# Kernel tuning notes

Hardware: AMD Instinct MI355X
Metric: run time of the kernel (lower is better)

Reference implementation:

```python
import jax, jax.numpy as jnp
import numpy as np

N_PTS = 2000   # n: number of Z1 samples (rows of K_Z1Z1)
Z_PTS = 2000   # z: number of Z2 samples (cols of K_Z1Z2 / gammas)
A_SAMP = 1000  # a: number of alpha samples
D = 8          # d: treatment dimension


def setup_inputs() -> dict:
    key = jax.random.key(0)
    ks = jax.random.split(key, 8)
    M = jax.random.normal(ks[0], (N_PTS, D), jnp.float32)
    N = jax.random.normal(ks[1], (N_PTS, D), jnp.float32)
    X = (M + N) / 2  # initial_X in the torch module (the nn.Parameter)
    # PSD kernel matrix so the ridge solve is well conditioned
    A = jax.random.normal(ks[2], (N_PTS, N_PTS), jnp.float32)
    K_Z1Z1 = (A @ A.T) / N_PTS
    K_Z1Z2 = jax.random.normal(ks[3], (N_PTS, Z_PTS), jnp.float32) * 0.1
    gamma_MN = jax.random.normal(ks[4], (N_PTS, Z_PTS), jnp.float32) * 0.01
    # offset keeps the complex denominator exps @ gamma_N away from zero
    gamma_N = jax.random.normal(ks[5], (N_PTS, Z_PTS), jnp.float32) * 0.01 + 1.0 / N_PTS
    alpha_samples = jax.random.normal(ks[6], (A_SAMP, D), jnp.float32)
    log_lambda_X = jnp.zeros((1,), jnp.float32)  # log(lambda_N) with lambda_N = 1.0
    return {
        "M": M, "N": N, "X": X, "log_lambda_X": log_lambda_X,
        "K_Z1Z1": K_Z1Z1, "K_Z1Z2": K_Z1Z2,
        "gamma_MN": gamma_MN, "gamma_N": gamma_N,
        "alpha_samples": alpha_samples,
    }


def _compute_labels(alpha, exponent, gamma_num, gamma_den, mult_num):
    # exps: [a, n] complex64 phase features exp(i * <alpha, exponent_j>)
    exps = jnp.exp(1j * (alpha @ exponent.T))
    # denominator: [a, z]
    denom = exps @ gamma_den.astype(jnp.complex64)
    # numerator: [a, z, d]
    num = jnp.einsum('jd,jz,aj->azd',
                     mult_num.astype(jnp.complex64),
                     gamma_num.astype(jnp.complex64),
                     exps)
    return num / denom[:, :, None]


def reference(M, N, X, log_lambda_X, K_Z1Z1, K_Z1Z2, gamma_MN, gamma_N, alpha_samples):
    n = K_Z1Z1.shape[0]
    # kernel ridge solve: gamma_X = (K + n*exp(log_lambda)*I)^{-1} K_Z1Z2  -> [n, z]
    reg = n * jnp.exp(log_lambda_X[0])
    gamma_X = jnp.linalg.solve(K_Z1Z1 + reg * jnp.eye(n, dtype=K_Z1Z1.dtype), K_Z1Z2)
    MN_labels = _compute_labels(alpha_samples, N, gamma_MN, gamma_N, M)   # [a, z, d]
    X_labels = _compute_labels(alpha_samples, X, gamma_X, gamma_X, X)     # [a, z, d]
    diff = MN_labels - X_labels
    # torch.linalg.norm(., dim=-1)**2 on complex == sum |.|^2 over d
    loss = jnp.mean(jnp.sum(jnp.abs(diff) ** 2, axis=-1))
    return loss
```

## Files before the change

### kernel.cpp

```cpp
#include <hip/hip_runtime.h>


typedef __bf16 bf16;
typedef __bf16 bf16x8 __attribute__((ext_vector_type(8)));
typedef float f32x4 __attribute__((ext_vector_type(4)));
typedef int i32x8 __attribute__((ext_vector_type(8)));

#define AS1 __attribute__((address_space(1)))
#define AS3 __attribute__((address_space(3)))

__device__ __forceinline__ void async16(const void* g, void* l) {
  __builtin_amdgcn_global_load_lds((AS1 const unsigned int*)g,
                                   (AS3 unsigned int*)l, 16, 0, 0);
}

__device__ __forceinline__ unsigned int pk4f8(float a, float b, float c,
                                              float d) {
  int w = __builtin_amdgcn_cvt_pk_fp8_f32(a, b, 0, false);
  w = __builtin_amdgcn_cvt_pk_fp8_f32(c, d, w, true);
  return (unsigned int)w;
}

__device__ __forceinline__ void build_mn(const float* __restrict__ gMN,
                                         const float* __restrict__ Mm,
                                         unsigned char* __restrict__ B8,
                                         int j0, int zl0, int zg0, int ZC,
                                         int tid, float (*t)[65]) {
  const size_t PL = (size_t)ZC * 2048;
  int zg = zg0 + zl0;
  for (int e = tid; e < 4096; e += 256) {
    int r = e >> 6, c = e & 63;
    t[r][c] = (j0 + r < 2000 && zg + c < 2000)
                  ? gMN[(size_t)(j0 + r) * 2000 + zg + c] : 0.f;
  }
  __syncthreads();
  const float4* M4 = (const float4*)Mm;
#pragma unroll
  for (int it = 0; it < 2; ++it) {
    int idx = it * 256 + tid;
    int zr = idx >> 3, c8 = (idx & 7) * 8;
    float g[8], mrow[8][8];
#pragma unroll
    for (int e = 0; e < 8; ++e) {
      g[e] = 64.f * t[c8 + e][zr];
      int jj = j0 + c8 + e;
      if (jj < 2000) {
        float4 ma = M4[jj * 2], mb = M4[jj * 2 + 1];
        mrow[e][0] = ma.x; mrow[e][1] = ma.y; mrow[e][2] = ma.z;
        mrow[e][3] = ma.w; mrow[e][4] = mb.x; mrow[e][5] = mb.y;
        mrow[e][6] = mb.z; mrow[e][7] = mb.w;
      } else {
#pragma unroll
        for (int d = 0; d < 8; ++d) mrow[e][d] = 0.f;
      }
    }
    size_t ob = (size_t)(zl0 + zr) * 2048 + j0 + c8;
#pragma unroll
    for (int d = 0; d < 8; ++d) {
      uint2 u;
      u.x = pk4f8(g[0] * mrow[0][d], g[1] * mrow[1][d], g[2] * mrow[2][d],
                  g[3] * mrow[3][d]);
      u.y = pk4f8(g[4] * mrow[4][d], g[5] * mrow[5][d], g[6] * mrow[6][d],
                  g[7] * mrow[7][d]);
      *(uint2*)(B8 + (size_t)d * PL + ob) = u;
    }
  }
}

__device__ __forceinline__ void build_x(const bf16* __restrict__ gxHi,
                                        const bf16* __restrict__ gxLo,
                                        const float* __restrict__ Xm,
                                        unsigned char* __restrict__ B8,
                                        int j0, int zl0, int zg0, int ZC,
                                        int tid) {
  const size_t PL = (size_t)ZC * 2048;
  const float4* X4 = (const float4*)Xm;
#pragma unroll
  for (int it = 0; it < 2; ++it) {
    int idx = it * 256 + tid;
    int zr = idx >> 3, c8 = (idx & 7) * 8;
    size_t gb = (size_t)(zg0 + zl0 + zr) * 2048 + j0 + c8;
    bf16x8 vh = *(const bf16x8*)(gxHi + gb);
    bf16x8 vl = *(const bf16x8*)(gxLo + gb);
    float gx[8], xr[8][8];
#pragma unroll
    for (int e = 0; e < 8; ++e) {
      gx[e] = 8192.f * ((float)vh[e] + (float)vl[e]);
      int jj = j0 + c8 + e;
      if (jj < 2000) {
        float4 xa = X4[jj * 2], xb = X4[jj * 2 + 1];
        xr[e][0] = xa.x; xr[e][1] = xa.y; xr[e][2] = xa.z; xr[e][3] = xa.w;
        xr[e][4] = xb.x; xr[e][5] = xb.y; xr[e][6] = xb.z; xr[e][7] = xb.w;
      } else {
#pragma unroll
        for (int d = 0; d < 8; ++d) xr[e][d] = 0.f;
      }
    }
    size_t ob = (size_t)(zl0 + zr) * 2048 + j0 + c8;
#pragma unroll
    for (int d = 0; d < 8; ++d) {
      uint2 u;
      u.x = pk4f8(gx[0] * xr[0][d], gx[1] * xr[1][d], gx[2] * xr[2][d],
                  gx[3] * xr[3][d]);
      u.y = pk4f8(gx[4] * xr[4][d], gx[5] * xr[5][d], gx[6] * xr[6][d],
                  gx[7] * xr[7][d]);
      *(uint2*)(B8 + (size_t)(8 + d) * PL + ob) = u;
    }
  }
}

__global__ __launch_bounds__(256) void k_cvt(
    const float* __restrict__ K11, const float* __restrict__ K12,
    const float* __restrict__ gN, bf16* __restrict__ Kbf,
    bf16* __restrict__ K12T, bf16* __restrict__ K12TL,
    bf16* __restrict__ BtNh, bf16* __restrict__ BtNl,
    float* __restrict__ out) {
  __shared__ float t[64][65];
  const int bid = blockIdx.x, tid = threadIdx.x;
  if (bid < 2048) {
    if (bid == 0 && tid == 0) out[0] = 0.f;
    int e = (bid * 256 + tid) * 8;
    int j = e >> 11, k = e & 2047;
    bf16x8 v;
    if (j < 2000 && k < 2000) {
      const float4* s = (const float4*)(K11 + (size_t)j * 2000 + k);
      float4 f0 = s[0], f1 = s[1];
      v[0] = (bf16)f0.x; v[1] = (bf16)f0.y; v[2] = (bf16)f0.z; v[3] = (bf16)f0.w;
      v[4] = (bf16)f1.x; v[5] = (bf16)f1.y; v[6] = (bf16)f1.z; v[7] = (bf16)f1.w;
    } else {
      for (int i = 0; i < 8; ++i) v[i] = (bf16)0.f;
    }
    *(bf16x8*)(Kbf + e) = v;
  } else {
    bool isK12 = bid < 3072;
    const float* src = isK12 ? K12 : gN;
    bf16* dh = isK12 ? K12T : BtNh;
    bf16* dl = isK12 ? K12TL : BtNl;
    int b2 = bid - (isK12 ? 2048 : 3072);
    int j0 = (b2 & 31) * 64, z0 = (b2 >> 5) * 64;
    for (int e = tid; e < 4096; e += 256) {
      int r = e >> 6, c = e & 63;
      t[r][c] = (j0 + r < 2000 && z0 + c < 2000)
                    ? src[(size_t)(j0 + r) * 2000 + z0 + c] : 0.f;
    }
    __syncthreads();
#pragma unroll
    for (int it = 0; it < 2; ++it) {
      int idx = it * 256 + tid;
      int zr = idx >> 3, c8 = (idx & 7) * 8;
      bf16x8 vh, vl;
#pragma unroll
      for (int e = 0; e < 8; ++e) {
        float g = t[c8 + e][zr];
        bf16 h = (bf16)g;
        vh[e] = h;
        vl[e] = (bf16)(g - (float)h);
      }
      size_t ob = (size_t)(z0 + zr) * 2048 + j0 + c8;
      *(bf16x8*)(dh + ob) = vh;
      *(bf16x8*)(dl + ob) = vl;
    }
  }
}

__global__ __launch_bounds__(256, 2) void k_big(
    const bf16* __restrict__ K12T, const bf16* __restrict__ K12TL,
    const bf16* __restrict__ Kbf, const float* __restrict__ ll,
    const float* __restrict__ al, const float* __restrict__ Nm,
    const float* __restrict__ Xm, const float* __restrict__ gMN,
    const float* __restrict__ Mm, bf16* __restrict__ gxHi,
    bf16* __restrict__ gxLo, bf16* __restrict__ AphH,
    bf16* __restrict__ AphL, unsigned char* __restrict__ Aph8,
    unsigned char* __restrict__ B8, int ZC) {
  __shared__ __align__(16) char smem[34816];
  const int tid = threadIdx.x;
  const int bid = blockIdx.x;
  if (bid >= 1280) {
    int pid = bid - 1280;
    build_mn(gMN, Mm, B8, (pid & 31) * 64, (pid >> 5) * 64, 0, ZC, tid,
             (float(*)[65])smem);
    return;
  }
  if (bid >= 256) {
    const size_t PA = (size_t)1024 * 2048;
    int a = bid - 256;
    int j0 = tid * 8;
    float vc[4][8];
    if (a < 1000) {
      const float4* A4 = (const float4*)al;
      const float4* N4 = (const float4*)Nm;
      const float4* X4 = (const float4*)Xm;
      float4 a0 = A4[a * 2], a1 = A4[a * 2 + 1];
#pragma unroll
      for (int e = 0; e < 8; ++e) {
        int j = j0 + e;
        if (j < 2000) {
          float4 n0 = N4[j * 2], n1 = N4[j * 2 + 1];
          float4 x0 = X4[j * 2], x1 = X4[j * 2 + 1];
          float pn = a0.x * n0.x + a0.y * n0.y + a0.z * n0.z + a0.w * n0.w +
                     a1.x * n1.x + a1.y * n1.y + a1.z * n1.z + a1.w * n1.w;
          float px = a0.x * x0.x + a0.y * x0.y + a0.z * x0.z + a0.w * x0.w +
                     a1.x * x1.x + a1.y * x1.y + a1.z * x1.z + a1.w * x1.w;
          __sincosf(pn, &vc[1][e], &vc[0][e]);
          __sincosf(px, &vc[3][e], &vc[2][e]);
        } else {
          vc[0][e] = vc[1][e] = vc[2][e] = vc[3][e] = 0.f;
        }
      }
    } else {
#pragma unroll
      for (int p = 0; p < 4; ++p)
#pragma unroll
        for (int e = 0; e < 8; ++e) vc[p][e] = 0.f;
    }
    size_t o = (size_t)a * 2048 + j0;
#pragma unroll
    for (int p = 0; p < 4; ++p) {
      bf16x8 vh, vl;
#pragma unroll
      for (int e = 0; e < 8; ++e) {
        bf16 h = (bf16)vc[p][e];
        vh[e] = h;
        vl[e] = (bf16)(vc[p][e] - (float)h);
      }
      *(bf16x8*)(AphH + p * PA + o) = vh;
      *(bf16x8*)(AphL + p * PA + o) = vl;
      uint2 u8;
      u8.x = pk4f8(vc[p][0], vc[p][1], vc[p][2], vc[p][3]);
      u8.y = pk4f8(vc[p][4], vc[p][5], vc[p][6], vc[p][7]);
      *(uint2*)(Aph8 + p * PA + o) = u8;
    }
    return;
  }
  bf16(*lds)[128][64] = (bf16(*)[128][64])smem;
  int bm = (bid >> 4) * 128;
  int bn = (bid & 15) * 128;
  const int w = tid >> 6, ln = tid & 63;
  const int r8 = ln >> 3, c8 = (ln & 7) * 8;
  f32x4 acc[4][4];
#pragma unroll
  for (int i = 0; i < 4; i++)
#pragma unroll
    for (int j = 0; j < 4; j++) acc[i][j] = {0.f, 0.f, 0.f, 0.f};
  const int m0 = (w & 1) * 64, n0 = (w >> 1) * 64;
  const int fr = ln & 15, kq = (ln >> 4) * 8;
  for (int kt = 0; kt < 2048; kt += 64) {
#pragma unroll
    for (int q = 0; q < 4; ++q) {
      int row = (w * 4 + q) * 8 + r8;
      async16(K12T + (size_t)(bm + row) * 2048 + (kt + c8), &lds[0][row][c8]);
      async16(Kbf + (size_t)(bn + row) * 2048 + (kt + c8), &lds[1][row][c8]);
    }
    __syncthreads();
#pragma unroll
    for (int ks = 0; ks < 64; ks += 32) {
      bf16x8 a[4], b[4];
#pragma unroll
      for (int i = 0; i < 4; i++) {
        a[i] = *(const bf16x8*)&lds[0][m0 + i * 16 + fr][ks + kq];
        b[i] = *(const bf16x8*)&lds[1][n0 + i * 16 + fr][ks + kq];
      }
#pragma unroll
      for (int i = 0; i < 4; i++)
#pragma unroll
        for (int j = 0; j < 4; j++)
          acc[i][j] = __builtin_amdgcn_mfma_f32_16x16x32_bf16(
              a[i], b[j], acc[i][j], 0, 0, 0);
    }
    __syncthreads();
  }
  float inv = 1.f / (2000.f * __expf(ll[0]));
  float* ft = (float*)smem;
  const int cr = (ln >> 4) * 4, cc = ln & 15;
  const int gtid = (tid & 7) * 8;
#pragma unroll
  for (int h = 0; h < 2; ++h) {
    if ((w >> 1) == h) {
#pragma unroll
      for (int i = 0; i < 4; i++)
#pragma unroll
        for (int j = 0; j < 4; j++)
#pragma unroll
          for (int r = 0; r < 4; r++)
            ft[(m0 + i * 16 + cr + r) * 68 + j * 16 + cc] = acc[i][j][r];
    }
    __syncthreads();
    int jbase = bn + h * 64 + gtid;
#pragma unroll
    for (int it = 0; it < 4; ++it) {
      int idx = it * 256 + tid;
      int m = idx >> 3;
      int zg = bm + m;
      size_t gb = (size_t)zg * 2048 + jbase;
      bf16x8 kh = *(const bf16x8*)(K12T + gb);
      bf16x8 klo = *(const bf16x8*)(K12TL + gb);
      bf16x8 vh, vl;
#pragma unroll
      for (int e = 0; e < 8; ++e) {
        float t1 = ft[m * 68 + gtid + e];
        float gx = ((float)kh[e] + (float)klo[e] - t1 * inv) * inv;
        bf16 hh = (bf16)gx;
        vh[e] = hh;
        vl[e] = (bf16)(gx - (float)hh);
      }
      *(bf16x8*)(gxHi + gb) = vh;
      *(bf16x8*)(gxLo + gb) = vl;
    }
    __syncthreads();
  }
}

__global__ __launch_bounds__(256) void k_prepX(
    const bf16* __restrict__ gxHi, const bf16* __restrict__ gxLo,
    const float* __restrict__ Xm, unsigned char* __restrict__ B8, int ZC) {
  int pid = blockIdx.x;
  build_x(gxHi, gxLo, Xm, B8, (pid & 31) * 64, (pid >> 5) * 64, 0, ZC,
          threadIdx.x);
}

__global__ __launch_bounds__(256, 2) void k_mm(
    const bf16* __restrict__ AphH, const bf16* __restrict__ AphL,
    const unsigned char* __restrict__ Aph8,
    const unsigned char* __restrict__ B8, const bf16* __restrict__ BtNh,
    const bf16* __restrict__ BtNl, const bf16* __restrict__ gxHi,
    const bf16* __restrict__ gxLo, unsigned int* __restrict__ Cpk,
    float* __restrict__ den, int ZC, int zg0) {
  const size_t PA = (size_t)1024 * 2048;
  const size_t PL8 = (size_t)ZC * 2048;
  const size_t PC = (size_t)1024 * ZC;
  __shared__ __align__(16) bf16 smem[3 * 128 * 64];
  const int tid = threadIdx.x;
  const int w = tid >> 6, ln = tid & 63;
  const int fr = ln & 15;
  const int cr = (ln >> 4) * 4, cc = ln & 15;
  const int zb = blockIdx.z;

  if (zb < 16) {
    unsigned char* l8 = (unsigned char*)smem;
    const unsigned char* A0 = Aph8 + (size_t)(zb < 8 ? 0 : 2) * PA;
    const unsigned char* A1 = A0 + PA;
    const unsigned char* B = B8 + (size_t)zb * PL8;
    const int sb = (zb < 8) ? 0x79797979 : 0x72727272;
    unsigned int* P = Cpk + (size_t)zb * PC;
    int bm = blockIdx.x * 128, bn = blockIdx.y * 128;
    const int colb = (ln & 7) * 16;
    const int kg = (ln >> 4) * 32;

    f32x4 acc0[4][4], acc1[4][4];
#pragma unroll
    for (int i = 0; i < 4; i++)
#pragma unroll
      for (int j = 0; j < 4; j++) {
        acc0[i][j] = {0.f, 0.f, 0.f, 0.f};
        acc1[i][j] = {0.f, 0.f, 0.f, 0.f};
      }
    const int m0 = (w & 1) * 64, n0 = (w >> 1) * 64;

    for (int kt = 0; kt < 2048; kt += 128) {
#pragma unroll
      for (int q = 0; q < 4; ++q) {
        int row = w * 32 + q * 8 + (ln >> 3);
        async16(A0 + (size_t)(bm + row) * 2048 + kt + colb,
                l8 + row * 128 + colb);
        async16(A1 + (size_t)(bm + row) * 2048 + kt + colb,
                l8 + 16384 + row * 128 + colb);
        async16(B + (size_t)(bn + row) * 2048 + kt + colb,
                l8 + 32768 + row * 128 + colb);
      }
      __syncthreads();
      i32x8 a0[4], a1[4];
#pragma unroll
      for (int i = 0; i < 4; i++) {
        a0[i] = *(const i32x8*)(l8 + (m0 + i * 16 + fr) * 128 + kg);
        a1[i] = *(const i32x8*)(l8 + 16384 + (m0 + i * 16 + fr) * 128 + kg);
      }
#pragma unroll
      for (int j = 0; j < 4; ++j) {
        i32x8 bf = *(const i32x8*)(l8 + 32768 + (n0 + j * 16 + fr) * 128 + kg);
#pragma unroll
        for (int i = 0; i < 4; ++i) {
          acc0[i][j] = __builtin_amdgcn_mfma_scale_f32_16x16x128_f8f6f4(
              a0[i], bf, acc0[i][j], 0, 0, 0, 0x7F7F7F7F, 0, sb);
          acc1[i][j] = __builtin_amdgcn_mfma_scale_f32_16x16x128_f8f6f4(
              a1[i], bf, acc1[i][j], 0, 0, 0, 0x7F7F7F7F, 0, sb);
        }
      }
      __syncthreads();
    }
#pragma unroll
    for (int i = 0; i < 4; i++)
#pragma unroll
      for (int j = 0; j < 4; j++)
#pragma unroll
        for (int r = 0; r < 4; r++) {
          union { bf16 h[2]; unsigned int u; } pk;
          pk.h[0] = (bf16)acc0[i][j][r];
          pk.h[1] = (bf16)acc1[i][j][r];
          P[(size_t)(bm + m0 + i * 16 + cr + r) * ZC +
            (bn + n0 + j * 16 + cc)] = pk.u;
        }
  } else {
    bf16(*lds)[64] = (bf16(*)[64])smem;
    const int kq = (ln >> 4) * 8;
    int nyTiles = ZC / 64;
    int den_idx = (zb - 16) * (ZC / 128) + blockIdx.y;
    int p = den_idx / nyTiles;
    int ny = den_idx % nyTiles;
    int side = p >> 1, trig = p & 1;
    const bf16* Ah = AphH + (size_t)(side * 2 + trig) * PA;
    const bf16* Al = AphL + (size_t)(side * 2 + trig) * PA;
    const bf16* Bh = (side ? gxHi : BtNh) + (size_t)zg0 * 2048;
    const bf16* Bl = (side ? gxLo : BtNl) + (size_t)zg0 * 2048;
    float* C = den + (size_t)p * PC;
    int bm = blockIdx.x * 128, bn = ny * 64;
    const int r32 = tid >> 3, c8 = (tid & 7) * 8;

    f32x4 acc[4][2];
#pragma unroll
    for (int i = 0; i < 4; i++)
#pragma unroll
      for (int j = 0; j < 2; j++) acc[i][j] = {0.f, 0.f, 0.f, 0.f};
    const int m0 = (w & 1) * 64, n0 = (w >> 1) * 32;

    for (int kt = 0; kt < 2048; kt += 64) {
#pragma unroll
      for (int q = 0; q < 4; ++q) {
        int row = q * 32 + r32;
        async16(Ah + (size_t)(bm + row) * 2048 + (kt + c8), &lds[row][c8]);
        async16(Al + (size_t)(bm + row) * 2048 + (kt + c8),
                &lds[128 + row][c8]);
      }
#pragma unroll
      for (int q = 0; q < 2; ++q) {
        int row = q * 32 + r32;
        async16(Bh + (size_t)(bn + row) * 2048 + (kt + c8),
                &lds[256 + row][c8]);
        async16(Bl + (size_t)(bn + row) * 2048 + (kt + c8),
                &lds[320 + row][c8]);
      }
      __syncthreads();
#pragma unroll
      for (int ks = 0; ks < 64; ks += 32) {
        bf16x8 ah[4], alo[4], bh[2], blo[2];
#pragma unroll
        for (int i = 0; i < 4; i++) {
          ah[i]  = *(const bf16x8*)&lds[m0 + i * 16 + fr][ks + kq];
          alo[i] = *(const bf16x8*)&lds[128 + m0 + i * 16 + fr][ks + kq];
        }
#pragma unroll
        for (int j = 0; j < 2; j++) {
          bh[j]  = *(const bf16x8*)&lds[256 + n0 + j * 16 + fr][ks + kq];
          blo[j] = *(const bf16x8*)&lds[320 + n0 + j * 16 + fr][ks + kq];
        }
#pragma unroll
        for (int i = 0; i < 4; i++)
#pragma unroll
          for (int j = 0; j < 2; j++) {
            acc[i][j] = __builtin_amdgcn_mfma_f32_16x16x32_bf16(
                alo[i], bh[j], acc[i][j], 0, 0, 0);
            acc[i][j] = __builtin_amdgcn_mfma_f32_16x16x32_bf16(
                ah[i], blo[j], acc[i][j], 0, 0, 0);
            acc[i][j] = __builtin_amdgcn_mfma_f32_16x16x32_bf16(
                ah[i], bh[j], acc[i][j], 0, 0, 0);
          }
      }
      __syncthreads();
    }
#pragma unroll
    for (int i = 0; i < 4; i++)
#pragma unroll
      for (int j = 0; j < 2; j++)
#pragma unroll
        for (int r = 0; r < 4; r++) {
          size_t idx = (size_t)(bm + m0 + i * 16 + cr + r) * ZC +
                       (bn + n0 + j * 16 + cc);
          C[idx] = acc[i][j][r];
        }
  }
}

__device__ __forceinline__ void load8p(const unsigned int* p, float* re,
                                       float* im) {
  uint4 u0 = ((const uint4*)p)[0], u1 = ((const uint4*)p)[1];
  re[0] = __uint_as_float(u0.x << 16); im[0] = __uint_as_float(u0.x & 0xffff0000u);
  re[1] = __uint_as_float(u0.y << 16); im[1] = __uint_as_float(u0.y & 0xffff0000u);
  re[2] = __uint_as_float(u0.z << 16); im[2] = __uint_as_float(u0.z & 0xffff0000u);
  re[3] = __uint_as_float(u0.w << 16); im[3] = __uint_as_float(u0.w & 0xffff0000u);
  re[4] = __uint_as_float(u1.x << 16); im[4] = __uint_as_float(u1.x & 0xffff0000u);
  re[5] = __uint_as_float(u1.y << 16); im[5] = __uint_as_float(u1.y & 0xffff0000u);
  re[6] = __uint_as_float(u1.z << 16); im[6] = __uint_as_float(u1.z & 0xffff0000u);
  re[7] = __uint_as_float(u1.w << 16); im[7] = __uint_as_float(u1.w & 0xffff0000u);
}
__device__ __forceinline__ void load8d(const float* p, float* o) {
  float4 f0 = ((const float4*)p)[0], f1 = ((const float4*)p)[1];
  o[0] = f0.x; o[1] = f0.y; o[2] = f0.z; o[3] = f0.w;
  o[4] = f1.x; o[5] = f1.y; o[6] = f1.z; o[7] = f1.w;
}

__global__ __launch_bounds__(256) void k_redprep(
    const unsigned int* __restrict__ Cpk, const float* __restrict__ den,
    float* __restrict__ out, const float* __restrict__ gMN,
    const float* __restrict__ Mm, const bf16* __restrict__ gxHi,
    const bf16* __restrict__ gxLo, const float* __restrict__ Xm,
    unsigned char* __restrict__ B8Next, int ZC, int zg0) {
  __shared__ float sm[64][65];
  const int bid = blockIdx.x, tid = threadIdx.x;
  if (bid >= 500) {
    int pid = bid - 500;
    int j0 = (pid & 31) * 64, zl0 = (pid >> 5) * 64;
    int zg0n = zg0 + ZC;
    build_mn(gMN, Mm, B8Next, j0, zl0, zg0n, ZC, tid, sm);
    build_x(gxHi, gxLo, Xm, B8Next, j0, zl0, zg0n, ZC, tid);
    return;
  }
  const size_t PS = (size_t)1024 * ZC;
  int a = bid * 2 + (tid >> 7);
  int zt = tid & 127;
  float acc = 0.f;
  for (int z = zt * 8; z < ZC; z += 1024) {
    if (zg0 + z >= 2000) break;
    size_t base = (size_t)a * ZC + z;
    float mdr[8], mdi[8], xdr[8], xdi[8], im[8], ix[8];
    load8d(den + 0 * PS + base, mdr);
    load8d(den + 1 * PS + base, mdi);
    load8d(den + 2 * PS + base, xdr);
    load8d(den + 3 * PS + base, xdi);
#pragma unroll
    for (int e = 0; e < 8; ++e) {
      im[e] = 1.f / (mdr[e] * mdr[e] + mdi[e] * mdi[e]);
      ix[e] = 1.f / (xdr[e] * xdr[e] + xdi[e] * xdi[e]);
    }
#pragma unroll
    for (int d = 0; d < 8; ++d) {
      float ar[8], ai[8], br[8], bi[8];
      load8p(Cpk + (size_t)d * PS + base, ar, ai);
      load8p(Cpk + (size_t)(8 + d) * PS + base, br, bi);
#pragma unroll
      for (int e = 0; e < 8; ++e) {
        float r1 = (ar[e] * mdr[e] + ai[e] * mdi[e]) * im[e];
        float i1 = (ai[e] * mdr[e] - ar[e] * mdi[e]) * im[e];
        float r2 = (br[e] * xdr[e] + bi[e] * xdi[e]) * ix[e];
        float i2 = (bi[e] * xdr[e] - br[e] * xdi[e]) * ix[e];
        float dr = r1 - r2, di = i1 - i2;
        acc += dr * dr + di * di;
      }
    }
  }
  for (int off = 32; off; off >>= 1) acc += __shfl_down(acc, off, 64);
  __shared__ float red[4];
  if (!(tid & 63)) red[tid >> 6] = acc;
  __syncthreads();
  if (!tid)
    atomicAdd(out, (red[0] + red[1] + red[2] + red[3]) * (1.f / 2000000.f));
}

extern "C" void kernel_launch(void* const* d_in, const int* in_sizes, int n_in,
                              void* d_out, int out_size, void* d_ws,
                              size_t ws_size, hipStream_t stream) {
  const float* Mm  = (const float*)d_in[0];
  const float* Nm  = (const float*)d_in[1];
  const float* Xm  = (const float*)d_in[2];
  const float* ll  = (const float*)d_in[3];
  const float* K11 = (const float*)d_in[4];
  const float* K12 = (const float*)d_in[5];
  const float* gMN = (const float*)d_in[6];
  const float* gN  = (const float*)d_in[7];
  const float* al  = (const float*)d_in[8];

  char* ws = (char*)d_ws;
  const size_t MB = 1024 * 1024;
  bf16* AphH = (bf16*)(ws);
  bf16* AphL = (bf16*)(ws + 16 * MB);
  unsigned char* Aph8 = (unsigned char*)(ws + 32 * MB);
  bf16* gxHi = (bf16*)(ws + 40 * MB);
  bf16* gxLo = (bf16*)(ws + 48 * MB);
  bf16* BtNh = (bf16*)(ws + 56 * MB);
  bf16* BtNl = (bf16*)(ws + 64 * MB);
  char* chunkRgn = ws + 72 * MB;

  size_t fixedNeed = 96 * MB;
  size_t avail = (ws_size > fixedNeed) ? ws_size - fixedNeed : 0;
  int ZC = 2048;
  while (ZC > 128 && (size_t)114688 * ZC > avail) ZC >>= 1;
  int NC = 2048 / ZC;
  unsigned char* B8c = (unsigned char*)(chunkRgn);
  float* denc = (float*)(chunkRgn + (size_t)32768 * ZC);
  unsigned int* Cpkc = (unsigned int*)(chunkRgn + (size_t)49152 * ZC);
  char* trans = chunkRgn + (size_t)114688 * ZC;
  bf16* Kbf   = (bf16*)(trans);
  bf16* K12T  = (bf16*)(trans + 8 * MB);
  bf16* K12TL = (bf16*)(trans + 16 * MB);

  int NBP = 32 * (ZC / 64);

  k_cvt<<<dim3(4096), dim3(256), 0, stream>>>(K11, K12, gN, Kbf, K12T, K12TL,
                                              BtNh, BtNl, (float*)d_out);
  k_big<<<dim3(1280 + NBP), dim3(256), 0, stream>>>(
      K12T, K12TL, Kbf, ll, al, Nm, Xm, gMN, Mm, gxHi, gxLo, AphH, AphL, Aph8,
      B8c, ZC);
  k_prepX<<<dim3(NBP), dim3(256), 0, stream>>>(gxHi, gxLo, Xm, B8c, ZC);
  for (int c = 0; c < NC; ++c) {
    int zg0 = c * ZC;
    k_mm<<<dim3(8, ZC / 128, 24), dim3(256), 0, stream>>>(
        AphH, AphL, Aph8, B8c, BtNh, BtNl, gxHi, gxLo, Cpkc, denc, ZC, zg0);
    int nblk = (c + 1 < NC) ? 500 + NBP : 500;
    k_redprep<<<dim3(nblk), dim3(256), 0, stream>>>(
        Cpkc, denc, (float*)d_out, gMN, Mm, gxHi, gxLo, Xm, B8c, ZC, zg0);
  }
  (void)in_sizes; (void)n_in; (void)out_size;
}
```

Baseline: 525.2 us.

## Swizzle LDS tiles, remap blocks to XCDs, and raise MFMA wave priority

Applies an XOR swizzle to the global-to-LDS copies and the matching LDS fragment reads in the solve GEMM and both k_mm paths, to avoid LDS bank conflicts. It also flattens the k_mm grid to 1D and maps blocks so each XCD works on related z-planes and tiles, which should improve L2 reuse. The k_big GEMM tiles are permuted the same way. s_setprio brackets the MFMA loops. The index remapping is intricate and relies on the mapping staying consistent with the grid size.

After: 457.7 us. 1.15x faster.

```diff
diff --git a/kernel.cpp b/kernel.cpp
--- a/kernel.cpp
+++ b/kernel.cpp
@@ -5,6 +5,7 @@
 typedef __bf16 bf16x8 __attribute__((ext_vector_type(8)));
 typedef float f32x4 __attribute__((ext_vector_type(4)));
 typedef int i32x8 __attribute__((ext_vector_type(8)));
+typedef int i32x4 __attribute__((ext_vector_type(4)));
 
 #define AS1 __attribute__((address_space(1)))
 #define AS3 __attribute__((address_space(3)))
@@ -19,6 +20,16 @@
   int w = __builtin_amdgcn_cvt_pk_fp8_f32(a, b, 0, false);
   w = __builtin_amdgcn_cvt_pk_fp8_f32(c, d, w, true);
   return (unsigned int)w;
+}
+
+__device__ __forceinline__ i32x8 ld_swz32(const unsigned char* rowp, int kg,
+                                          int fsw) {
+  i32x4 lo = *(const i32x4*)(rowp + (kg ^ fsw));
+  i32x4 hi = *(const i32x4*)(rowp + ((kg + 16) ^ fsw));
+  i32x8 v;
+  v[0] = lo[0]; v[1] = lo[1]; v[2] = lo[2]; v[3] = lo[3];
+  v[4] = hi[0]; v[5] = hi[1]; v[6] = hi[2]; v[7] = hi[3];
+  return v;
 }
 
 __device__ __forceinline__ void build_mn(const float* __restrict__ gMN,
@@ -233,8 +244,9 @@
     return;
   }
   bf16(*lds)[128][64] = (bf16(*)[128][64])smem;
-  int bm = (bid >> 4) * 128;
-  int bn = (bid & 15) * 128;
+  int wrk = (bid & 7) * 32 + (bid >> 3);
+  int bm = (wrk >> 4) * 128;
+  int bn = (wrk & 15) * 128;
   const int w = tid >> 6, ln = tid & 63;
   const int r8 = ln >> 3, c8 = (ln & 7) * 8;
   f32x4 acc[4][4];
@@ -244,12 +256,14 @@
     for (int j = 0; j < 4; j++) acc[i][j] = {0.f, 0.f, 0.f, 0.f};
   const int m0 = (w & 1) * 64, n0 = (w >> 1) * 64;
   const int fr = ln & 15, kq = (ln >> 4) * 8;
+  const int esw = (fr & 7) << 3;
   for (int kt = 0; kt < 2048; kt += 64) {
 #pragma unroll
     for (int q = 0; q < 4; ++q) {
       int row = (w * 4 + q) * 8 + r8;
-      async16(K12T + (size_t)(bm + row) * 2048 + (kt + c8), &lds[0][row][c8]);
-      async16(Kbf + (size_t)(bn + row) * 2048 + (kt + c8), &lds[1][row][c8]);
+      int sc = c8 ^ ((row & 7) << 3);
+      async16(K12T + (size_t)(bm + row) * 2048 + (kt + sc), &lds[0][row][c8]);
+      async16(Kbf + (size_t)(bn + row) * 2048 + (kt + sc), &lds[1][row][c8]);
     }
     __syncthreads();
 #pragma unroll
@@ -257,15 +271,17 @@
       bf16x8 a[4], b[4];
 #pragma unroll
       for (int i = 0; i < 4; i++) {
-        a[i] = *(const bf16x8*)&lds[0][m0 + i * 16 + fr][ks + kq];
-        b[i] = *(const bf16x8*)&lds[1][n0 + i * 16 + fr][ks + kq];
-      }
+        a[i] = *(const bf16x8*)&lds[0][m0 + i * 16 + fr][(ks + kq) ^ esw];
+        b[i] = *(const bf16x8*)&lds[1][n0 + i * 16 + fr][(ks + kq) ^ esw];
+      }
+      __builtin_amdgcn_s_setprio(1);
 #pragma unroll
       for (int i = 0; i < 4; i++)
 #pragma unroll
         for (int j = 0; j < 4; j++)
           acc[i][j] = __builtin_amdgcn_mfma_f32_16x16x32_bf16(
               a[i], b[j], acc[i][j], 0, 0, 0);
+      __builtin_amdgcn_s_setprio(0);
     }
     __syncthreads();
   }
@@ -333,18 +349,29 @@
   const int w = tid >> 6, ln = tid & 63;
   const int fr = ln & 15;
   const int cr = (ln >> 4) * 4, cc = ln & 15;
-  const int zb = blockIdx.z;
-
-  if (zb < 16) {
+
+  const int BYT = ZC >> 7;
+  const int nyT = ZC >> 6;
+  const int xcd = blockIdx.x & 7;
+  const int slot = blockIdx.x >> 3;
+  const int numSlots = 16 * BYT;
+
+  if (slot < numSlots) {
+    const int half = numSlots >> 1;
+    int zb = xcd * 2 + (slot >= half ? 1 : 0);
+    int rem = slot & (half - 1);
+    int bn = (rem >> 3) * 128;
+    int bm = (rem & 7) * 128;
+
     unsigned char* l8 = (unsigned char*)smem;
     const unsigned char* A0 = Aph8 + (size_t)(zb < 8 ? 0 : 2) * PA;
     const unsigned char* A1 = A0 + PA;
     const unsigned char* B = B8 + (size_t)zb * PL8;
     const int sb = (zb < 8) ? 0x79797979 : 0x72727272;
     unsigned int* P = Cpk + (size_t)zb * PC;
-    int bm = blockIdx.x * 128, bn = blockIdx.y * 128;
     const int colb = (ln & 7) * 16;
     const int kg = (ln >> 4) * 32;
+    const int fsw = (fr & 7) << 4;
 
     f32x4 acc0[4][4], acc1[4][4];
 #pragma unroll
@@ -360,31 +387,36 @@
 #pragma unroll
       for (int q = 0; q < 4; ++q) {
         int row = w * 32 + q * 8 + (ln >> 3);
-        async16(A0 + (size_t)(bm + row) * 2048 + kt + colb,
+        int sc = colb ^ ((row & 7) << 4);
+        async16(A0 + (size_t)(bm + row) * 2048 + kt + sc,
                 l8 + row * 128 + colb);
-        async16(A1 + (size_t)(bm + row) * 2048 + kt + colb,
+        async16(A1 + (size_t)(bm + row) * 2048 + kt + sc,
                 l8 + 16384 + row * 128 + colb);
-        async16(B + (size_t)(bn + row) * 2048 + kt + colb,
+        async16(B + (size_t)(bn + row) * 2048 + kt + sc,
                 l8 + 32768 + row * 128 + colb);
       }
       __syncthreads();
       i32x8 a0[4], a1[4];
 #pragma unroll
       for (int i = 0; i < 4; i++) {
-        a0[i] = *(const i32x8*)(l8 + (m0 + i * 16 + fr) * 128 + kg);
-        a1[i] = *(const i32x8*)(l8 + 16384 + (m0 + i * 16 + fr) * 128 + kg);
-      }
+        const unsigned char* pr = l8 + (m0 + i * 16 + fr) * 128;
+        a0[i] = ld_swz32(pr, kg, fsw);
+        a1[i] = ld_swz32(pr + 16384, kg, fsw);
+      }
+      __builtin_amdgcn_s_setprio(1);
 #pragma unroll
       for (int j = 0; j < 4; ++j) {
-        i32x8 bf = *(const i32x8*)(l8 + 32768 + (n0 + j * 16 + fr) * 128 + kg);
+        i32x8 bfv =
+            ld_swz32(l8 + 32768 + (n0 + j * 16 + fr) * 128, kg, fsw);
 #pragma unroll
         for (int i = 0; i < 4; ++i) {
           acc0[i][j] = __builtin_amdgcn_mfma_scale_f32_16x16x128_f8f6f4(
-              a0[i], bf, acc0[i][j], 0, 0, 0, 0x7F7F7F7F, 0, sb);
+              a0[i], bfv, acc0[i][j], 0, 0, 0, 0x7F7F7F7F, 0, sb);
           acc1[i][j] = __builtin_amdgcn_mfma_scale_f32_16x16x128_f8f6f4(
-              a1[i], bf, acc1[i][j], 0, 0, 0, 0x7F7F7F7F, 0, sb);
+              a1[i], bfv, acc1[i][j], 0, 0, 0, 0x7F7F7F7F, 0, sb);
         }
       }
+      __builtin_amdgcn_s_setprio(0);
       __syncthreads();
     }
 #pragma unroll
@@ -402,40 +434,42 @@
   } else {
     bf16(*lds)[64] = (bf16(*)[64])smem;
     const int kq = (ln >> 4) * 8;
-    int nyTiles = ZC / 64;
-    int den_idx = (zb - 16) * (ZC / 128) + blockIdx.y;
-    int p = den_idx / nyTiles;
-    int ny = den_idx % nyTiles;
+    const int esw = (fr & 7) << 3;
+    int j = slot - numSlots;
+    int p = xcd >> 1;
+    int ny = (xcd & 1) * (nyT >> 1) + (j >> 3);
     int side = p >> 1, trig = p & 1;
     const bf16* Ah = AphH + (size_t)(side * 2 + trig) * PA;
     const bf16* Al = AphL + (size_t)(side * 2 + trig) * PA;
     const bf16* Bh = (side ? gxHi : BtNh) + (size_t)zg0 * 2048;
     const bf16* Bl = (side ? gxLo : BtNl) + (size_t)zg0 * 2048;
     float* C = den + (size_t)p * PC;
-    int bm = blockIdx.x * 128, bn = ny * 64;
+    int bm = (j & 7) * 128, bn = ny * 64;
     const int r32 = tid >> 3, c8 = (tid & 7) * 8;
 
     f32x4 acc[4][2];
 #pragma unroll
     for (int i = 0; i < 4; i++)
 #pragma unroll
-      for (int j = 0; j < 2; j++) acc[i][j] = {0.f, 0.f, 0.f, 0.f};
+      for (int jj = 0; jj < 2; jj++) acc[i][jj] = {0.f, 0.f, 0.f, 0.f};
     const int m0 = (w & 1) * 64, n0 = (w >> 1) * 32;
 
     for (int kt = 0; kt < 2048; kt += 64) {
 #pragma unroll
       for (int q = 0; q < 4; ++q) {
         int row = q * 32 + r32;
-        async16(Ah + (size_t)(bm + row) * 2048 + (kt + c8), &lds[row][c8]);
-        async16(Al + (size_t)(bm + row) * 2048 + (kt + c8),
+        int sc = c8 ^ ((row & 7) << 3);
+        async16(Ah + (size_t)(bm + row) * 2048 + (kt + sc), &lds[row][c8]);
+        async16(Al + (size_t)(bm + row) * 2048 + (kt + sc),
                 &lds[128 + row][c8]);
       }
 #pragma unroll
       for (int q = 0; q < 2; ++q) {
         int row = q * 32 + r32;
-        async16(Bh + (size_t)(bn + row) * 2048 + (kt + c8),
+        int sc = c8 ^ ((row & 7) << 3);
+        async16(Bh + (size_t)(bn + row) * 2048 + (kt + sc),
                 &lds[256 + row][c8]);
-        async16(Bl + (size_t)(bn + row) * 2048 + (kt + c8),
+        async16(Bl + (size_t)(bn + row) * 2048 + (kt + sc),
                 &lds[320 + row][c8]);
       }
       __syncthreads();
@@ -444,37 +478,42 @@
         bf16x8 ah[4], alo[4], bh[2], blo[2];
 #pragma unroll
         for (int i = 0; i < 4; i++) {
-          ah[i]  = *(const bf16x8*)&lds[m0 + i * 16 + fr][ks + kq];
-          alo[i] = *(const bf16x8*)&lds[128 + m0 + i * 16 + fr][ks + kq];
+          ah[i]  = *(const bf16x8*)&lds[m0 + i * 16 + fr][(ks + kq) ^ esw];
+          alo[i] =
+              *(const bf16x8*)&lds[128 + m0 + i * 16 + fr][(ks + kq) ^ esw];
         }
 #pragma unroll
-        for (int j = 0; j < 2; j++) {
-          bh[j]  = *(const bf16x8*)&lds[256 + n0 + j * 16 + fr][ks + kq];
-          blo[j] = *(const bf16x8*)&lds[320 + n0 + j * 16 + fr][ks + kq];
+        for (int jj = 0; jj < 2; jj++) {
+          bh[jj] =
+              *(const bf16x8*)&lds[256 + n0 + jj * 16 + fr][(ks + kq) ^ esw];
+          blo[jj] =
+              *(const bf16x8*)&lds[320 + n0 + jj * 16 + fr][(ks + kq) ^ esw];
         }
+        __builtin_amdgcn_s_setprio(1);
 #pragma unroll
         for (int i = 0; i < 4; i++)
 #pragma unroll
-          for (int j = 0; j < 2; j++) {
-            acc[i][j] = __builtin_amdgcn_mfma_f32_16x16x32_bf16(
-                alo[i], bh[j], acc[i][j], 0, 0, 0);
-            acc[i][j] = __builtin_amdgcn_mfma_f32_16x16x32_bf16(
-                ah[i], blo[j], acc[i][j], 0, 0, 0);
-            acc[i][j] = __builtin_amdgcn_mfma_f32_16x16x32_bf16(
-                ah[i], bh[j], acc[i][j], 0, 0, 0);
+          for (int jj = 0; jj < 2; jj++) {
+            acc[i][jj] = __builtin_amdgcn_mfma_f32_16x16x32_bf16(
+                alo[i], bh[jj], acc[i][jj], 0, 0, 0);
+            acc[i][jj] = __builtin_amdgcn_mfma_f32_16x16x32_bf16(
+                ah[i], blo[jj], acc[i][jj], 0, 0, 0);
+            acc[i][jj] = __builtin_amdgcn_mfma_f32_16x16x32_bf16(
+                ah[i], bh[jj], acc[i][jj], 0, 0, 0);
           }
+        __builtin_amdgcn_s_setprio(0);
       }
       __syncthreads();
     }
 #pragma unroll
     for (int i = 0; i < 4; i++)
 #pragma unroll
-      for (int j = 0; j < 2; j++)
+      for (int jj = 0; jj < 2; jj++)
 #pragma unroll
         for (int r = 0; r < 4; r++) {
           size_t idx = (size_t)(bm + m0 + i * 16 + cr + r) * ZC +
-                       (bn + n0 + j * 16 + cc);
-          C[idx] = acc[i][j][r];
+                       (bn + n0 + jj * 16 + cc);
+          C[idx] = acc[i][jj][r];
         }
   }
 }
@@ -592,6 +631,7 @@
   bf16* K12TL = (bf16*)(trans + 16 * MB);
 
   int NBP = 32 * (ZC / 64);
+  int GMM = 192 * (ZC >> 7);
 
   k_cvt<<<dim3(4096), dim3(256), 0, stream>>>(K11, K12, gN, Kbf, K12T, K12TL,
                                               BtNh, BtNl, (float*)d_out);
@@ -601,7 +641,7 @@
   k_prepX<<<dim3(NBP), dim3(256), 0, stream>>>(gxHi, gxLo, Xm, B8c, ZC);
   for (int c = 0; c < NC; ++c) {
     int zg0 = c * ZC;
-    k_mm<<<dim3(8, ZC / 128, 24), dim3(256), 0, stream>>>(
+    k_mm<<<dim3(GMM), dim3(256), 0, stream>>>(
         AphH, AphL, Aph8, B8c, BtNh, BtNl, gxHi, gxLo, Cpkc, denc, ZC, zg0);
     int nblk = (c + 1 < NC) ? 500 + NBP : 500;
     k_redprep<<<dim3(nblk), dim3(256), 0, stream>>>(
```
